# Kernel tuning notes

Hardware: AMD Instinct MI355X
Metric: run time of the kernel (lower is better)

The kernel has to match this reference:

```python
import jax, jax.numpy as jnp
import numpy as np

B, L, FD, G = 256, 512, 64, 32
H1, H2, DH = 512, 512, 256  # leaf_hidden=[512,512], diffuse_hidden=[256]

def _gelu(x):
    return jax.nn.gelu(x, approximate=False)  # torch nn.GELU default (erf)

def setup_inputs() -> dict:
    key = jax.random.key(0)
    ks = jax.random.split(key, 14)
    def lin(k, fan_in, shape):
        s = 1.0 / np.sqrt(fan_in)
        return jax.random.uniform(k, shape, jnp.float32, -s, s)
    return {
        "Xg": jax.random.normal(ks[0], (B, G), jnp.float32),
        "Xl": jax.random.normal(ks[1], (B, L, FD), jnp.float32),
        "W1": lin(ks[2], FD, (FD, H1)), "b1": lin(ks[3], FD, (H1,)),
        "W2": lin(ks[4], H1, (H1, H2)), "b2": lin(ks[5], H1, (H2,)),
        "wa": lin(ks[6], H2, (H2, 1)), "ba": lin(ks[7], H2, (1,)),
        "wt": lin(ks[8], H2, (H2, 1)), "bt": lin(ks[9], H2, (1,)),
        "Wd1": lin(ks[10], G + H2, (G + H2, DH)), "bd1": lin(ks[11], G + H2, (DH,)),
        "Wd2": lin(ks[12], DH, (DH, 1)), "bd2": lin(ks[13], DH, (1,)),
    }

def reference(Xg, Xl, W1, b1, W2, b2, wa, ba, wt, bt, Wd1, bd1, Wd2, bd2):
    # per-leaf MLP encoder: [B, L, FD] -> [B, L, H2]
    h = _gelu(jnp.einsum("blf,fh->blh", Xl, W1) + b1)
    h = _gelu(jnp.einsum("blh,hk->blk", h, W2) + b2)
    absorb = jax.nn.softplus(jnp.einsum("blh,ho->bl", h, wa) + ba[0])  # [B, L]
    atten = jax.nn.softplus(jnp.einsum("blh,ho->bl", h, wt) + bt[0])   # [B, L]
    # flip bottom->top to top->bottom
    absorb_tb = absorb[:, ::-1]
    atten_tb = atten[:, ::-1]
    # T_i = prod_{j<i} exp(-atten_tb_j) = exp(-exclusive_cumsum(atten_tb))
    excl = jnp.cumsum(atten_tb, axis=1) - atten_tb
    T = jnp.exp(-excl)
    captured = jnp.sum(T * absorb_tb, axis=1, keepdims=True)  # [B, 1]
    pooled = jnp.mean(h, axis=1)  # [B, H2]
    z = jnp.concatenate([Xg, pooled], axis=1)
    d = _gelu(z @ Wd1 + bd1) @ Wd2 + bd2  # [B, 1]
    return captured + d
```

## Files before the change

kernel.cpp:

```cpp
#include <hip/hip_runtime.h>
#include <hip/hip_bf16.h>
#include <math.h>

#define B_SZ   256
#define L_SZ   512
#define FD_SZ  64
#define H1_SZ  512
#define H2_SZ  512
#define G_SZ   32
#define DH_SZ  256
#define M_SZ   (B_SZ * L_SZ)

typedef __bf16 bfx8 __attribute__((ext_vector_type(8)));
typedef __bf16 bfx4 __attribute__((ext_vector_type(4)));
typedef float  f32x4 __attribute__((ext_vector_type(4)));
typedef float  f32x16 __attribute__((ext_vector_type(16)));

__device__ __forceinline__ float gelu_exact(float x) {
  return 0.5f * x * (1.0f + erff(x * 0.70710678118654752440f));
}
__device__ __forceinline__ float gelu_fast(float x) {
  float x2 = x * x;
  float w = x * fmaf(0.102943398f, x2, 2.30220931f);
  float e = __builtin_amdgcn_exp2f(-w);
  return x * __builtin_amdgcn_rcpf(1.0f + e);
}
__device__ __forceinline__ float softplus_f(float x) {
  return (x > 20.0f) ? x : log1pf(expf(x));
}
__device__ __forceinline__ __bf16 f2bf(float f) { return (__bf16)f; }

#define ROR_ADD(x, n)                                                          \
  {                                                                            \
    int _t = __builtin_amdgcn_mov_dpp(__builtin_bit_cast(int, (x)),            \
                                      0x120 + (n), 0xF, 0xF, true);            \
    (x) += __builtin_bit_cast(float, _t);                                      \
  }

#define MFMA16(a, b, c) __builtin_amdgcn_mfma_f32_16x16x32_bf16((a), (b), (c), 0, 0, 0)
#define MFMA32(a, b, c) __builtin_amdgcn_mfma_f32_32x32x16_bf16((a), (b), (c), 0, 0, 0)

__global__ void repack_kernel(const float* __restrict__ W1,
                              const float* __restrict__ W2,
                              __bf16* __restrict__ W1p,
                              __bf16* __restrict__ W2p,
                              float* __restrict__ pooled) {
  int t = blockIdx.x * 256 + threadIdx.x;
  if (t < 32768)
    *reinterpret_cast<float4*>(pooled + (size_t)t * 4) = (float4){0.f, 0.f, 0.f, 0.f};
  if (t < 4096) {
    int lane = t & 63, blk = t >> 6;
    int ks = blk & 1, mb = blk >> 1;
    int col = 16 * mb + (lane & 15);
    int kbase = ks * 32 + (lane >> 4) * 8;
    bfx8 o;
#pragma unroll
    for (int j = 0; j < 8; ++j) o[j] = f2bf(W1[(size_t)(kbase + j) * H1_SZ + col]);
    *reinterpret_cast<bfx8*>(W1p + (size_t)t * 8) = o;
  } else if (t < 4096 + 32768) {
    int t2 = t - 4096;
    int lane = t2 & 63, blk = t2 >> 6;
    int ks = blk & 31, nb = blk >> 5;
    int col = 32 * nb + (lane & 31);
    int kbase = 16 * ks + (lane >> 5) * 8;
    bfx8 o;
#pragma unroll
    for (int j = 0; j < 8; ++j) o[j] = f2bf(W2[(size_t)(kbase + j) * H2_SZ + col]);
    *reinterpret_cast<bfx8*>(W2p + (size_t)t2 * 8) = o;
  }
}

__global__ __launch_bounds__(512, 4) void fused_kernel(
    const float* __restrict__ Xl,
    const __bf16* __restrict__ W1p, const __bf16* __restrict__ W2p,
    const float* __restrict__ b1, const float* __restrict__ b2,
    const float* __restrict__ wa, const float* __restrict__ ba,
    const float* __restrict__ wt, const float* __restrict__ bt,
    float* __restrict__ absorbW, float* __restrict__ attenW,
    float* __restrict__ pooled) {
  __shared__ __bf16 Xs[64 * 64];
  __shared__ __bf16 H1s[64 * 512];
  __shared__ float sl[8 * 64 * 2];

  const int tid = threadIdx.x;
  const int lane = tid & 63;
  const int w = tid >> 6;
  const int g = lane >> 4;
  const int c = lane & 15;
  const int c32 = lane & 31;
  const int kg = lane >> 5;
  const int R0 = blockIdx.x * 64;
  const int bidx = R0 >> 9;

#pragma unroll
  for (int i = 0; i < 2; ++i) {
    int idx = i * 512 + tid;
    int r = idx >> 4;
    int c4 = idx & 15;
    float4 v = *reinterpret_cast<const float4*>(Xl + (size_t)(R0 + r) * FD_SZ + c4 * 4);
    bfx4 bv;
    bv[0] = f2bf(v.x); bv[1] = f2bf(v.y); bv[2] = f2bf(v.z); bv[3] = f2bf(v.w);
    int chunk = c4 >> 1;
    int off = r * 64 + (((chunk ^ (r & 7)) << 3) + (c4 & 1) * 4);
    *reinterpret_cast<bfx4*>(&Xs[off]) = bv;
  }
  __syncthreads();

  f32x4 acc1[4][4];
#pragma unroll
  for (int mi = 0; mi < 4; ++mi)
#pragma unroll
    for (int ni = 0; ni < 4; ++ni) acc1[mi][ni] = (f32x4){0.f, 0.f, 0.f, 0.f};

#pragma unroll
  for (int ks = 0; ks < 2; ++ks) {
    bfx8 a1[4];
#pragma unroll
    for (int mi = 0; mi < 4; ++mi) {
      int mb = 4 * w + mi;
      a1[mi] = *reinterpret_cast<const bfx8*>(W1p + ((size_t)(mb * 2 + ks) * 64 + lane) * 8);
    }
    bfx8 bx[4];
#pragma unroll
    for (int ni = 0; ni < 4; ++ni) {
      int r = 16 * ni + c;
      int chunk = ks * 4 + g;
      bx[ni] = *reinterpret_cast<const bfx8*>(&Xs[r * 64 + ((chunk ^ (r & 7)) << 3)]);
    }
#pragma unroll
    for (int mi = 0; mi < 4; ++mi)
#pragma unroll
      for (int ni = 0; ni < 4; ++ni)
        acc1[mi][ni] = MFMA16(a1[mi], bx[ni], acc1[mi][ni]);
  }

#pragma unroll
  for (int mi = 0; mi < 4; ++mi) {
    int mb = 4 * w + mi;
    float4 bias4 = *reinterpret_cast<const float4*>(b1 + 16 * mb + 4 * g);
#pragma unroll
    for (int ni = 0; ni < 4; ++ni) {
      int r = 16 * ni + c;
      bfx4 pv;
      pv[0] = f2bf(gelu_fast(acc1[mi][ni][0] + bias4.x));
      pv[1] = f2bf(gelu_fast(acc1[mi][ni][1] + bias4.y));
      pv[2] = f2bf(gelu_fast(acc1[mi][ni][2] + bias4.z));
      pv[3] = f2bf(gelu_fast(acc1[mi][ni][3] + bias4.w));
      int kchunk = 2 * mb + (g >> 1);
      int off = r * 512 + ((kchunk ^ (r & 31)) << 3) + (g & 1) * 4;
      *reinterpret_cast<bfx4*>(&H1s[off]) = pv;
    }
  }
  __syncthreads();

  f32x16 acc2[2][2];
#pragma unroll
  for (int m = 0; m < 2; ++m)
#pragma unroll
    for (int n = 0; n < 2; ++n)
#pragma unroll
      for (int q = 0; q < 16; ++q) acc2[m][n][q] = 0.0f;

  const __bf16* wpb = W2p + ((size_t)(2 * w) * 32 * 64 + lane) * 8;
  for (int ks = 0; ks < 32; ++ks) {
    bfx8 a2[2];
#pragma unroll
    for (int m = 0; m < 2; ++m) {
      int r = 32 * m + c32;
      int chunk = 2 * ks + kg;
      a2[m] = *reinterpret_cast<const bfx8*>(&H1s[r * 512 + ((chunk ^ (r & 31)) << 3)]);
    }
    bfx8 bw0 = *reinterpret_cast<const bfx8*>(wpb + (size_t)ks * 512);
    bfx8 bw1 = *reinterpret_cast<const bfx8*>(wpb + (size_t)16384 + ks * 512);
    __builtin_amdgcn_s_setprio(1);
    acc2[0][0] = MFMA32(a2[0], bw0, acc2[0][0]);
    acc2[0][1] = MFMA32(a2[0], bw1, acc2[0][1]);
    acc2[1][0] = MFMA32(a2[1], bw0, acc2[1][0]);
    acc2[1][1] = MFMA32(a2[1], bw1, acc2[1][1]);
    __builtin_amdgcn_s_setprio(0);
  }

  float b2v[2], wav[2], wtv[2];
#pragma unroll
  for (int n = 0; n < 2; ++n) {
    int col = 32 * (2 * w + n) + c32;
    b2v[n] = b2[col];
    wav[n] = wa[col];
    wtv[n] = wt[col];
  }
  float pool0 = 0.0f, pool1 = 0.0f;
  const int rbase = 4 * kg;

#pragma unroll
  for (int m = 0; m < 2; ++m) {
#pragma unroll
    for (int reg = 0; reg < 16; ++reg) {
      float v0 = gelu_fast(acc2[m][0][reg] + b2v[0]);
      float v1 = gelu_fast(acc2[m][1][reg] + b2v[1]);
      float sa = v0 * wav[0] + v1 * wav[1];
      float st = v0 * wtv[0] + v1 * wtv[1];
      pool0 += v0;
      pool1 += v1;
      ROR_ADD(sa, 8); ROR_ADD(sa, 4); ROR_ADD(sa, 2); ROR_ADD(sa, 1);
      ROR_ADD(st, 8); ROR_ADD(st, 4); ROR_ADD(st, 2); ROR_ADD(st, 1);
      sa += __shfl_xor(sa, 16, 64);
      st += __shfl_xor(st, 16, 64);
      if (c32 == 0) {
        int row = 32 * m + (reg & 3) + 8 * (reg >> 2) + rbase;
        float2 v2 = make_float2(sa, st);
        *reinterpret_cast<float2*>(&sl[w * 128 + row * 2]) = v2;
      }
    }
  }
  pool0 += __shfl_xor(pool0, 32, 64);
  pool1 += __shfl_xor(pool1, 32, 64);
  if (lane < 32) {
    atomicAdd(&pooled[bidx * H2_SZ + 32 * (2 * w)     + c32], pool0);
    atomicAdd(&pooled[bidx * H2_SZ + 32 * (2 * w + 1) + c32], pool1);
  }
  __syncthreads();

  if (tid < 64) {
    float sa = 0.0f, st = 0.0f;
#pragma unroll
    for (int w8 = 0; w8 < 8; ++w8) {
      float2 v2 = *reinterpret_cast<float2*>(&sl[w8 * 128 + tid * 2]);
      sa += v2.x; st += v2.y;
    }
    absorbW[R0 + tid] = softplus_f(sa + ba[0]);
    attenW[R0 + tid]  = softplus_f(st + bt[0]);
  }
}

__global__ __launch_bounds__(256) void finalize_kernel(
    const float* __restrict__ Xg,
    const float* __restrict__ absorbW, const float* __restrict__ attenW,
    const float* __restrict__ pooled,
    const float* __restrict__ Wd1, const float* __restrict__ bd1,
    const float* __restrict__ Wd2, const float* __restrict__ bd2,
    float* __restrict__ out) {
  __shared__ float s0[512];
  __shared__ float s1[512];
  __shared__ float sab[512];
  __shared__ float zz[544];
  __shared__ float redc[4];
  __shared__ float redd[4];

  const int b = blockIdx.x;
  const int t = threadIdx.x;
  const int i0 = t, i1 = t + 256;

  float a0 = attenW[b * L_SZ + (L_SZ - 1 - i0)];
  float a1 = attenW[b * L_SZ + (L_SZ - 1 - i1)];
  sab[i0] = absorbW[b * L_SZ + (L_SZ - 1 - i0)];
  sab[i1] = absorbW[b * L_SZ + (L_SZ - 1 - i1)];
  s0[i0] = a0; s0[i1] = a1;
  __syncthreads();

  float* src = s0;
  float* dst = s1;
  for (int off = 1; off < 512; off <<= 1) {
    float v0 = src[i0] + ((i0 >= off) ? src[i0 - off] : 0.0f);
    float v1 = src[i1] + ((i1 >= off) ? src[i1 - off] : 0.0f);
    dst[i0] = v0; dst[i1] = v1;
    __syncthreads();
    float* tmp = src; src = dst; dst = tmp;
  }

  float p = expf(-(src[i0] - a0)) * sab[i0] + expf(-(src[i1] - a1)) * sab[i1];
#pragma unroll
  for (int off = 32; off; off >>= 1) p += __shfl_down(p, off, 64);
  if ((t & 63) == 0) redc[t >> 6] = p;

  if (t < G_SZ) zz[t] = Xg[b * G_SZ + t];
  zz[G_SZ + i0] = pooled[b * H2_SZ + i0] * (1.0f / (float)L_SZ);
  zz[G_SZ + i1] = pooled[b * H2_SZ + i1] * (1.0f / (float)L_SZ);
  __syncthreads();

  float s = bd1[t];
  for (int cc = 0; cc < G_SZ + H2_SZ; ++cc) s = fmaf(zz[cc], Wd1[cc * DH_SZ + t], s);
  float v = gelu_exact(s) * Wd2[t];
#pragma unroll
  for (int off = 32; off; off >>= 1) v += __shfl_down(v, off, 64);
  if ((t & 63) == 0) redd[t >> 6] = v;
  __syncthreads();

  if (t == 0) {
    float captured = redc[0] + redc[1] + redc[2] + redc[3];
    float d = redd[0] + redd[1] + redd[2] + redd[3] + bd2[0];
    out[b] = captured + d;
  }
}

extern "C" void kernel_launch(void* const* d_in, const int* in_sizes, int n_in,
                              void* d_out, int out_size, void* d_ws, size_t ws_size,
                              hipStream_t stream) {
  const float* Xg  = (const float*)d_in[0];
  const float* Xl  = (const float*)d_in[1];
  const float* W1  = (const float*)d_in[2];
  const float* b1  = (const float*)d_in[3];
  const float* W2  = (const float*)d_in[4];
  const float* b2  = (const float*)d_in[5];
  const float* wa  = (const float*)d_in[6];
  const float* ba  = (const float*)d_in[7];
  const float* wt  = (const float*)d_in[8];
  const float* bt  = (const float*)d_in[9];
  const float* Wd1 = (const float*)d_in[10];
  const float* bd1 = (const float*)d_in[11];
  const float* Wd2 = (const float*)d_in[12];
  const float* bd2 = (const float*)d_in[13];

  char* ws = (char*)d_ws;
  __bf16* W1p    = (__bf16*)(ws + 0);
  __bf16* W2p    = (__bf16*)(ws + 65536);
  float* absorbW = (float*)(ws + 589824);
  float* attenW  = (float*)(ws + 1114112);
  float* pooled  = (float*)(ws + 1638400);

  repack_kernel<<<144, 256, 0, stream>>>(W1, W2, W1p, W2p, pooled);
  fused_kernel<<<M_SZ / 64, 512, 0, stream>>>(Xl, W1p, W2p, b1, b2, wa, ba, wt, bt,
                                              absorbW, attenW, pooled);
  finalize_kernel<<<B_SZ, 256, 0, stream>>>(Xg, absorbW, attenW, pooled,
                                            Wd1, bd1, Wd2, bd2, (float*)d_out);
}
```

Baseline: 140.1 us.

## Fuse finalize into encoder via last-block-per-batch counter and pair reductions

Removes the separate finalize kernel launch. Each batch's eighth (last-arriving) block, detected with an atomic counter reset in the repack kernel, performs the transmittance scan, pooled MLP head and output write, reusing shared memory. The epilogue row reduction is also restructured to process two rows per shuffle step by swapping halves across lanes, halving the DPP/shuffle reduction count. Adds threadfence and atomic overhead per block and serializes finalize work on a few late blocks.

```diff
diff --git a/kernel.cpp b/kernel.cpp
--- a/kernel.cpp
+++ b/kernel.cpp
@@ -44,8 +44,10 @@
                               const float* __restrict__ W2,
                               __bf16* __restrict__ W1p,
                               __bf16* __restrict__ W2p,
-                              float* __restrict__ pooled) {
+                              float* __restrict__ pooled,
+                              int* __restrict__ cnt) {
   int t = blockIdx.x * 256 + threadIdx.x;
+  if (t < B_SZ) cnt[t] = 0;
   if (t < 32768)
     *reinterpret_cast<float4*>(pooled + (size_t)t * 4) = (float4){0.f, 0.f, 0.f, 0.f};
   if (t < 4096) {
@@ -71,16 +73,20 @@
 }
 
 __global__ __launch_bounds__(512, 4) void fused_kernel(
-    const float* __restrict__ Xl,
+    const float* __restrict__ Xg, const float* __restrict__ Xl,
     const __bf16* __restrict__ W1p, const __bf16* __restrict__ W2p,
     const float* __restrict__ b1, const float* __restrict__ b2,
     const float* __restrict__ wa, const float* __restrict__ ba,
     const float* __restrict__ wt, const float* __restrict__ bt,
+    const float* __restrict__ Wd1, const float* __restrict__ bd1,
+    const float* __restrict__ Wd2, const float* __restrict__ bd2,
     float* __restrict__ absorbW, float* __restrict__ attenW,
-    float* __restrict__ pooled) {
+    float* __restrict__ pooled, int* __restrict__ cnt,
+    float* __restrict__ out) {
   __shared__ __bf16 Xs[64 * 64];
   __shared__ __bf16 H1s[64 * 512];
   __shared__ float sl[8 * 64 * 2];
+  __shared__ int lastflag;
 
   const int tid = threadIdx.x;
   const int lane = tid & 63;
@@ -190,25 +196,39 @@
   }
   float pool0 = 0.0f, pool1 = 0.0f;
   const int rbase = 4 * kg;
+  const bool hi16 = (lane & 16) != 0;
 
 #pragma unroll
   for (int m = 0; m < 2; ++m) {
 #pragma unroll
-    for (int reg = 0; reg < 16; ++reg) {
-      float v0 = gelu_fast(acc2[m][0][reg] + b2v[0]);
-      float v1 = gelu_fast(acc2[m][1][reg] + b2v[1]);
-      float sa = v0 * wav[0] + v1 * wav[1];
-      float st = v0 * wtv[0] + v1 * wtv[1];
-      pool0 += v0;
-      pool1 += v1;
-      ROR_ADD(sa, 8); ROR_ADD(sa, 4); ROR_ADD(sa, 2); ROR_ADD(sa, 1);
-      ROR_ADD(st, 8); ROR_ADD(st, 4); ROR_ADD(st, 2); ROR_ADD(st, 1);
-      sa += __shfl_xor(sa, 16, 64);
-      st += __shfl_xor(st, 16, 64);
+    for (int q = 0; q < 8; ++q) {
+      int rA = 2 * q, rB = 2 * q + 1;
+      float v0a = gelu_fast(acc2[m][0][rA] + b2v[0]);
+      float v1a = gelu_fast(acc2[m][1][rA] + b2v[1]);
+      float v0b = gelu_fast(acc2[m][0][rB] + b2v[0]);
+      float v1b = gelu_fast(acc2[m][1][rB] + b2v[1]);
+      pool0 += v0a + v0b;
+      pool1 += v1a + v1b;
+      float saA = v0a * wav[0] + v1a * wav[1];
+      float saB = v0b * wav[0] + v1b * wav[1];
+      float stA = v0a * wtv[0] + v1a * wtv[1];
+      float stB = v0b * wtv[0] + v1b * wtv[1];
+      float zs = hi16 ? saB : saA;
+      float ys = hi16 ? saA : saB;
+      float zt = hi16 ? stB : stA;
+      float yt = hi16 ? stA : stB;
+      ys = __shfl_xor(ys, 16, 64);
+      yt = __shfl_xor(yt, 16, 64);
+      float ss = zs + ys;
+      float tt = zt + yt;
+      ROR_ADD(ss, 8); ROR_ADD(ss, 4); ROR_ADD(ss, 2); ROR_ADD(ss, 1);
+      ROR_ADD(tt, 8); ROR_ADD(tt, 4); ROR_ADD(tt, 2); ROR_ADD(tt, 1);
       if (c32 == 0) {
-        int row = 32 * m + (reg & 3) + 8 * (reg >> 2) + rbase;
-        float2 v2 = make_float2(sa, st);
-        *reinterpret_cast<float2*>(&sl[w * 128 + row * 2]) = v2;
+        int row = 32 * m + (rA & 3) + 8 * (rA >> 2) + rbase;
+        *reinterpret_cast<float2*>(&sl[w * 128 + row * 2]) = make_float2(ss, tt);
+      } else if (c32 == 16) {
+        int row = 32 * m + (rB & 3) + 8 * (rB >> 2) + rbase;
+        *reinterpret_cast<float2*>(&sl[w * 128 + row * 2]) = make_float2(ss, tt);
       }
     }
   }
@@ -230,65 +250,64 @@
     absorbW[R0 + tid] = softplus_f(sa + ba[0]);
     attenW[R0 + tid]  = softplus_f(st + bt[0]);
   }
-}
-
-__global__ __launch_bounds__(256) void finalize_kernel(
-    const float* __restrict__ Xg,
-    const float* __restrict__ absorbW, const float* __restrict__ attenW,
-    const float* __restrict__ pooled,
-    const float* __restrict__ Wd1, const float* __restrict__ bd1,
-    const float* __restrict__ Wd2, const float* __restrict__ bd2,
-    float* __restrict__ out) {
-  __shared__ float s0[512];
-  __shared__ float s1[512];
-  __shared__ float sab[512];
-  __shared__ float zz[544];
-  __shared__ float redc[4];
-  __shared__ float redd[4];
-
-  const int b = blockIdx.x;
-  const int t = threadIdx.x;
-  const int i0 = t, i1 = t + 256;
-
-  float a0 = attenW[b * L_SZ + (L_SZ - 1 - i0)];
-  float a1 = attenW[b * L_SZ + (L_SZ - 1 - i1)];
-  sab[i0] = absorbW[b * L_SZ + (L_SZ - 1 - i0)];
-  sab[i1] = absorbW[b * L_SZ + (L_SZ - 1 - i1)];
-  s0[i0] = a0; s0[i1] = a1;
+  __syncthreads();
+
+  if (tid == 0) {
+    __threadfence();
+    lastflag = (atomicAdd(&cnt[bidx], 1) == 7);
+  }
+  __syncthreads();
+  if (!lastflag) return;
+  __threadfence();
+
+  float* F   = reinterpret_cast<float*>(H1s);
+  float* s0  = F;
+  float* s1  = F + 512;
+  float* sab = F + 1024;
+  float* zz  = F + 1536;
+  float* redc = sl;
+  float* redd = sl + 16;
+
+  float av   = attenW[bidx * L_SZ + (L_SZ - 1 - tid)];
+  float sabv = absorbW[bidx * L_SZ + (L_SZ - 1 - tid)];
+  s0[tid] = av;
+  sab[tid] = sabv;
+  zz[G_SZ + tid] = pooled[bidx * H2_SZ + tid] * (1.0f / (float)L_SZ);
+  if (tid < G_SZ) zz[tid] = Xg[bidx * G_SZ + tid];
   __syncthreads();
 
   float* src = s0;
   float* dst = s1;
   for (int off = 1; off < 512; off <<= 1) {
-    float v0 = src[i0] + ((i0 >= off) ? src[i0 - off] : 0.0f);
-    float v1 = src[i1] + ((i1 >= off) ? src[i1 - off] : 0.0f);
-    dst[i0] = v0; dst[i1] = v1;
+    dst[tid] = src[tid] + ((tid >= off) ? src[tid - off] : 0.0f);
     __syncthreads();
     float* tmp = src; src = dst; dst = tmp;
   }
 
-  float p = expf(-(src[i0] - a0)) * sab[i0] + expf(-(src[i1] - a1)) * sab[i1];
+  float p = __expf(-(src[tid] - av)) * sabv;
 #pragma unroll
   for (int off = 32; off; off >>= 1) p += __shfl_down(p, off, 64);
-  if ((t & 63) == 0) redc[t >> 6] = p;
-
-  if (t < G_SZ) zz[t] = Xg[b * G_SZ + t];
-  zz[G_SZ + i0] = pooled[b * H2_SZ + i0] * (1.0f / (float)L_SZ);
-  zz[G_SZ + i1] = pooled[b * H2_SZ + i1] * (1.0f / (float)L_SZ);
-  __syncthreads();
-
-  float s = bd1[t];
-  for (int cc = 0; cc < G_SZ + H2_SZ; ++cc) s = fmaf(zz[cc], Wd1[cc * DH_SZ + t], s);
-  float v = gelu_exact(s) * Wd2[t];
-#pragma unroll
-  for (int off = 32; off; off >>= 1) v += __shfl_down(v, off, 64);
-  if ((t & 63) == 0) redd[t >> 6] = v;
-  __syncthreads();
-
-  if (t == 0) {
-    float captured = redc[0] + redc[1] + redc[2] + redc[3];
-    float d = redd[0] + redd[1] + redd[2] + redd[3] + bd2[0];
-    out[b] = captured + d;
+  if (lane == 0) redc[w] = p;
+
+  float dv = 0.0f;
+  if (tid < DH_SZ) {
+    float acc0 = bd1[tid], accb = 0.0f;
+    for (int cc = 0; cc < G_SZ + H2_SZ; cc += 2) {
+      acc0 = fmaf(zz[cc],     Wd1[(size_t)cc * DH_SZ + tid],       acc0);
+      accb = fmaf(zz[cc + 1], Wd1[(size_t)(cc + 1) * DH_SZ + tid], accb);
+    }
+    dv = gelu_exact(acc0 + accb) * Wd2[tid];
+  }
+#pragma unroll
+  for (int off = 32; off; off >>= 1) dv += __shfl_down(dv, off, 64);
+  if (lane == 0) redd[w] = dv;
+  __syncthreads();
+
+  if (tid == 0) {
+    float captured = 0.0f, d = bd2[0];
+#pragma unroll
+    for (int i = 0; i < 8; ++i) { captured += redc[i]; d += redd[i]; }
+    out[bidx] = captured + d;
   }
 }
 
@@ -316,10 +335,11 @@
   float* absorbW = (float*)(ws + 589824);
   float* attenW  = (float*)(ws + 1114112);
   float* pooled  = (float*)(ws + 1638400);
-
-  repack_kernel<<<144, 256, 0, stream>>>(W1, W2, W1p, W2p, pooled);
-  fused_kernel<<<M_SZ / 64, 512, 0, stream>>>(Xl, W1p, W2p, b1, b2, wa, ba, wt, bt,
-                                              absorbW, attenW, pooled);
-  finalize_kernel<<<B_SZ, 256, 0, stream>>>(Xg, absorbW, attenW, pooled,
-                                            Wd1, bd1, Wd2, bd2, (float*)d_out);
-}
+  int*   cnt     = (int*)(ws + 2162688);
+
+  repack_kernel<<<144, 256, 0, stream>>>(W1, W2, W1p, W2p, pooled, cnt);
+  fused_kernel<<<M_SZ / 64, 512, 0, stream>>>(Xg, Xl, W1p, W2p, b1, b2, wa, ba,
+                                              wt, bt, Wd1, bd1, Wd2, bd2,
+                                              absorbW, attenW, pooled, cnt,
+                                              (float*)d_out);
+}
```

Measured after the change: 391.4 us. +179.4%, slower.

## Double fused-kernel block to 1024 threads, halving per-wave tile and reduction work

Applied to the files above, without the earlier changes.

The fused MLP kernel now runs 16 waves per block instead of 8. Each wave owns half as many output columns in both GEMMs, with fewer accumulators and one W2 fragment per k-step. The row-wise dot-product reduction is also restructured: paired registers are exchanged across the half-wave with select+shuffle, so each butterfly reduction handles two rows at once. The intent is more latency hiding and fewer cross-lane ops per output. The cost is more waves contending for the same LDS tile and more partial sums to combine at the end.

```diff
diff --git a/kernel.cpp b/kernel.cpp
--- a/kernel.cpp
+++ b/kernel.cpp
@@ -70,7 +70,7 @@
   }
 }
 
-__global__ __launch_bounds__(512, 4) void fused_kernel(
+__global__ __launch_bounds__(1024, 8) void fused_kernel(
     const float* __restrict__ Xl,
     const __bf16* __restrict__ W1p, const __bf16* __restrict__ W2p,
     const float* __restrict__ b1, const float* __restrict__ b2,
@@ -80,7 +80,7 @@
     float* __restrict__ pooled) {
   __shared__ __bf16 Xs[64 * 64];
   __shared__ __bf16 H1s[64 * 512];
-  __shared__ float sl[8 * 64 * 2];
+  __shared__ float sl[16 * 64 * 2];
 
   const int tid = threadIdx.x;
   const int lane = tid & 63;
@@ -92,9 +92,8 @@
   const int R0 = blockIdx.x * 64;
   const int bidx = R0 >> 9;
 
-#pragma unroll
-  for (int i = 0; i < 2; ++i) {
-    int idx = i * 512 + tid;
+  {
+    int idx = tid;
     int r = idx >> 4;
     int c4 = idx & 15;
     float4 v = *reinterpret_cast<const float4*>(Xl + (size_t)(R0 + r) * FD_SZ + c4 * 4);
@@ -106,18 +105,18 @@
   }
   __syncthreads();
 
-  f32x4 acc1[4][4];
-#pragma unroll
-  for (int mi = 0; mi < 4; ++mi)
+  f32x4 acc1[2][4];
+#pragma unroll
+  for (int mi = 0; mi < 2; ++mi)
 #pragma unroll
     for (int ni = 0; ni < 4; ++ni) acc1[mi][ni] = (f32x4){0.f, 0.f, 0.f, 0.f};
 
 #pragma unroll
   for (int ks = 0; ks < 2; ++ks) {
-    bfx8 a1[4];
-#pragma unroll
-    for (int mi = 0; mi < 4; ++mi) {
-      int mb = 4 * w + mi;
+    bfx8 a1[2];
+#pragma unroll
+    for (int mi = 0; mi < 2; ++mi) {
+      int mb = 2 * w + mi;
       a1[mi] = *reinterpret_cast<const bfx8*>(W1p + ((size_t)(mb * 2 + ks) * 64 + lane) * 8);
     }
     bfx8 bx[4];
@@ -128,15 +127,15 @@
       bx[ni] = *reinterpret_cast<const bfx8*>(&Xs[r * 64 + ((chunk ^ (r & 7)) << 3)]);
     }
 #pragma unroll
-    for (int mi = 0; mi < 4; ++mi)
+    for (int mi = 0; mi < 2; ++mi)
 #pragma unroll
       for (int ni = 0; ni < 4; ++ni)
         acc1[mi][ni] = MFMA16(a1[mi], bx[ni], acc1[mi][ni]);
   }
 
 #pragma unroll
-  for (int mi = 0; mi < 4; ++mi) {
-    int mb = 4 * w + mi;
+  for (int mi = 0; mi < 2; ++mi) {
+    int mb = 2 * w + mi;
     float4 bias4 = *reinterpret_cast<const float4*>(b1 + 16 * mb + 4 * g);
 #pragma unroll
     for (int ni = 0; ni < 4; ++ni) {
@@ -153,15 +152,13 @@
   }
   __syncthreads();
 
-  f32x16 acc2[2][2];
+  f32x16 acc2[2];
 #pragma unroll
   for (int m = 0; m < 2; ++m)
 #pragma unroll
-    for (int n = 0; n < 2; ++n)
-#pragma unroll
-      for (int q = 0; q < 16; ++q) acc2[m][n][q] = 0.0f;
-
-  const __bf16* wpb = W2p + ((size_t)(2 * w) * 32 * 64 + lane) * 8;
+    for (int q = 0; q < 16; ++q) acc2[m][q] = 0.0f;
+
+  const __bf16* wpb = W2p + ((size_t)w * 32 * 64 + lane) * 8;
   for (int ks = 0; ks < 32; ++ks) {
     bfx8 a2[2];
 #pragma unroll
@@ -170,61 +167,60 @@
       int chunk = 2 * ks + kg;
       a2[m] = *reinterpret_cast<const bfx8*>(&H1s[r * 512 + ((chunk ^ (r & 31)) << 3)]);
     }
-    bfx8 bw0 = *reinterpret_cast<const bfx8*>(wpb + (size_t)ks * 512);
-    bfx8 bw1 = *reinterpret_cast<const bfx8*>(wpb + (size_t)16384 + ks * 512);
+    bfx8 bw = *reinterpret_cast<const bfx8*>(wpb + (size_t)ks * 512);
     __builtin_amdgcn_s_setprio(1);
-    acc2[0][0] = MFMA32(a2[0], bw0, acc2[0][0]);
-    acc2[0][1] = MFMA32(a2[0], bw1, acc2[0][1]);
-    acc2[1][0] = MFMA32(a2[1], bw0, acc2[1][0]);
-    acc2[1][1] = MFMA32(a2[1], bw1, acc2[1][1]);
+    acc2[0] = MFMA32(a2[0], bw, acc2[0]);
+    acc2[1] = MFMA32(a2[1], bw, acc2[1]);
     __builtin_amdgcn_s_setprio(0);
   }
 
-  float b2v[2], wav[2], wtv[2];
-#pragma unroll
-  for (int n = 0; n < 2; ++n) {
-    int col = 32 * (2 * w + n) + c32;
-    b2v[n] = b2[col];
-    wav[n] = wa[col];
-    wtv[n] = wt[col];
-  }
-  float pool0 = 0.0f, pool1 = 0.0f;
+  const int col = 32 * w + c32;
+  const float b2v = b2[col];
+  const float wav = wa[col];
+  const float wtv = wt[col];
+  float pool0 = 0.0f;
   const int rbase = 4 * kg;
+  const bool hi16 = (lane & 16) != 0;
 
 #pragma unroll
   for (int m = 0; m < 2; ++m) {
 #pragma unroll
-    for (int reg = 0; reg < 16; ++reg) {
-      float v0 = gelu_fast(acc2[m][0][reg] + b2v[0]);
-      float v1 = gelu_fast(acc2[m][1][reg] + b2v[1]);
-      float sa = v0 * wav[0] + v1 * wav[1];
-      float st = v0 * wtv[0] + v1 * wtv[1];
-      pool0 += v0;
-      pool1 += v1;
-      ROR_ADD(sa, 8); ROR_ADD(sa, 4); ROR_ADD(sa, 2); ROR_ADD(sa, 1);
-      ROR_ADD(st, 8); ROR_ADD(st, 4); ROR_ADD(st, 2); ROR_ADD(st, 1);
-      sa += __shfl_xor(sa, 16, 64);
-      st += __shfl_xor(st, 16, 64);
+    for (int q = 0; q < 8; ++q) {
+      int rA = 2 * q, rB = 2 * q + 1;
+      float vA = gelu_fast(acc2[m][rA] + b2v);
+      float vB = gelu_fast(acc2[m][rB] + b2v);
+      pool0 += vA + vB;
+      float saA = vA * wav, saB = vB * wav;
+      float stA = vA * wtv, stB = vB * wtv;
+      float zs = hi16 ? saB : saA;
+      float ys = hi16 ? saA : saB;
+      float zt = hi16 ? stB : stA;
+      float yt = hi16 ? stA : stB;
+      ys = __shfl_xor(ys, 16, 64);
+      yt = __shfl_xor(yt, 16, 64);
+      float ss = zs + ys;
+      float tt = zt + yt;
+      ROR_ADD(ss, 8); ROR_ADD(ss, 4); ROR_ADD(ss, 2); ROR_ADD(ss, 1);
+      ROR_ADD(tt, 8); ROR_ADD(tt, 4); ROR_ADD(tt, 2); ROR_ADD(tt, 1);
       if (c32 == 0) {
-        int row = 32 * m + (reg & 3) + 8 * (reg >> 2) + rbase;
-        float2 v2 = make_float2(sa, st);
-        *reinterpret_cast<float2*>(&sl[w * 128 + row * 2]) = v2;
+        int row = 32 * m + (rA & 3) + 8 * (rA >> 2) + rbase;
+        *reinterpret_cast<float2*>(&sl[w * 128 + row * 2]) = make_float2(ss, tt);
+      } else if (c32 == 16) {
+        int row = 32 * m + (rB & 3) + 8 * (rB >> 2) + rbase;
+        *reinterpret_cast<float2*>(&sl[w * 128 + row * 2]) = make_float2(ss, tt);
       }
     }
   }
   pool0 += __shfl_xor(pool0, 32, 64);
-  pool1 += __shfl_xor(pool1, 32, 64);
-  if (lane < 32) {
-    atomicAdd(&pooled[bidx * H2_SZ + 32 * (2 * w)     + c32], pool0);
-    atomicAdd(&pooled[bidx * H2_SZ + 32 * (2 * w + 1) + c32], pool1);
-  }
+  if (lane < 32)
+    atomicAdd(&pooled[bidx * H2_SZ + 32 * w + c32], pool0);
   __syncthreads();
 
   if (tid < 64) {
     float sa = 0.0f, st = 0.0f;
 #pragma unroll
-    for (int w8 = 0; w8 < 8; ++w8) {
-      float2 v2 = *reinterpret_cast<float2*>(&sl[w8 * 128 + tid * 2]);
+    for (int w16 = 0; w16 < 16; ++w16) {
+      float2 v2 = *reinterpret_cast<float2*>(&sl[w16 * 128 + tid * 2]);
       sa += v2.x; st += v2.y;
     }
     absorbW[R0 + tid] = softplus_f(sa + ba[0]);
@@ -318,8 +314,8 @@
   float* pooled  = (float*)(ws + 1638400);
 
   repack_kernel<<<144, 256, 0, stream>>>(W1, W2, W1p, W2p, pooled);
-  fused_kernel<<<M_SZ / 64, 512, 0, stream>>>(Xl, W1p, W2p, b1, b2, wa, ba, wt, bt,
-                                              absorbW, attenW, pooled);
+  fused_kernel<<<M_SZ / 64, 1024, 0, stream>>>(Xl, W1p, W2p, b1, b2, wa, ba,
+                                               wt, bt, absorbW, attenW, pooled);
   finalize_kernel<<<B_SZ, 256, 0, stream>>>(Xg, absorbW, attenW, pooled,
                                             Wd1, bd1, Wd2, bd2, (float*)d_out);
 }
```

New measurement: 140.7 us. About the same (+0.5%).
